# Optimization experiments

Measured on AMD Instinct MI355X. Metric: run time of the kernel, lower is better.

## Reference

```python
import jax, jax.numpy as jnp
import numpy as np

B, T, D = 8, 2048, 1024


def setup_inputs() -> dict:
    key = jax.random.key(0)
    ks = jax.random.split(key, 9)
    s = 1.0 / np.sqrt(D)
    return {
        "e": jax.random.normal(ks[0], (B, T, D), jnp.float32),
        "residual": jax.random.normal(ks[1], (B, T, D), jnp.float32),
        "Wq_w": jax.random.normal(ks[2], (D, D), jnp.float32) * s,
        "Wq_b": jax.random.normal(ks[3], (D,), jnp.float32) * s,
        "Wk_w": jax.random.normal(ks[4], (D, D), jnp.float32) * s,
        "Wk_b": jax.random.normal(ks[5], (D,), jnp.float32) * s,
        "Wv_w": jax.random.normal(ks[6], (D, D), jnp.float32) * s,
        "Wv_b": jax.random.normal(ks[7], (D,), jnp.float32) * s,
        "v_table": jax.random.normal(ks[8], (T, 1), jnp.float32),
    }


def reference(e, residual, Wq_w, Wq_b, Wk_w, Wk_b, Wv_w, Wv_b, v_table):
    T_ = e.shape[1]
    # relative position index: pos[i,j] = max(i - j, 0)
    pos = jnp.arange(T_)
    rel = jnp.maximum(pos[:, None] - pos[None, :], 0)          # (T, T) int
    pos_embd = v_table[rel, 0]                                 # (T, T) gather from Embedding(length, 1)

    # torch Linear: x @ W.T + b
    Q = e @ Wq_w.T + Wq_b                                      # (B, T, D)
    K = residual @ Wk_w.T + Wk_b                               # (B, T, D)
    V = e @ Wv_w.T + Wv_b                                      # (B, T, D)

    # Q @ K^T  (torch: Q @ Wk(residual).transpose(-2,-1))
    scores = jnp.einsum('btd,bsd->bts', Q, K)                  # (B, T, T)
    # einsum('BeT,Tt->BTt', K^T, pos_embd) == sum_e K[B,T,e] * pos_embd[T,t]
    scores = scores + K.sum(-1)[:, :, None] * pos_embd[None]   # (B, T, T)

    # causal mask via tril (zeros strictly-upper entries); NO softmax in this variant
    scores = scores * jnp.tril(jnp.ones((T_, T_), scores.dtype))
    return scores @ V                                          # (B, T, D)
```

## Files before the change

kernel.cpp:

```cpp
#include <hip/hip_runtime.h>

typedef unsigned short u16;
typedef __attribute__((ext_vector_type(8))) short bf16x8;
typedef __attribute__((ext_vector_type(8))) unsigned short u16x8;
typedef __attribute__((ext_vector_type(4))) float f32x4;

#define AS1 __attribute__((address_space(1)))
#define AS3 __attribute__((address_space(3)))

static __device__ __forceinline__ u16 f2bf(float f) {
  unsigned u = __float_as_uint(f);
  u += 0x7FFFu + ((u >> 16) & 1u);
  return (u16)(u >> 16);
}
static __device__ __forceinline__ float bf2f(u16 h) {
  return __uint_as_float(((unsigned)h) << 16);
}

__global__ __launch_bounds__(256) void conv_big(const float* __restrict__ e,
                                                const float* __restrict__ res,
                                                u16* __restrict__ eb, u16* __restrict__ rb) {
  int i = blockIdx.x * 256 + threadIdx.x;
  const float* in = blockIdx.z ? res : e;
  u16* out = blockIdx.z ? rb : eb;
  const float4* p = (const float4*)in + (size_t)i * 2;
  float4 a = p[0], b = p[1];
  u16x8 r;
  r[0] = f2bf(a.x); r[1] = f2bf(a.y); r[2] = f2bf(a.z); r[3] = f2bf(a.w);
  r[4] = f2bf(b.x); r[5] = f2bf(b.y); r[6] = f2bf(b.z); r[7] = f2bf(b.w);
  ((u16x8*)out)[i] = r;
}
__global__ __launch_bounds__(256) void conv_w(const float* __restrict__ w0,
                                              const float* __restrict__ w1,
                                              const float* __restrict__ w2,
                                              u16* __restrict__ o0, u16* __restrict__ o1,
                                              u16* __restrict__ o2,
                                              float* __restrict__ ksum) {
  int i = blockIdx.x * 256 + threadIdx.x;
  if (blockIdx.z == 3) {
    if (i < 16384) ksum[i] = 0.f;
    return;
  }
  const float* in = blockIdx.z == 0 ? w0 : (blockIdx.z == 1 ? w1 : w2);
  u16* out = blockIdx.z == 0 ? o0 : (blockIdx.z == 1 ? o1 : o2);
  const float4* p = (const float4*)in + (size_t)i * 2;
  float4 a = p[0], b = p[1];
  u16x8 r;
  r[0] = f2bf(a.x); r[1] = f2bf(a.y); r[2] = f2bf(a.z); r[3] = f2bf(a.w);
  r[4] = f2bf(b.x); r[5] = f2bf(b.y); r[6] = f2bf(b.z); r[7] = f2bf(b.w);
  ((u16x8*)out)[i] = r;
}

enum { M_BIASN = 0, M_BIASM = 1, M_SCORES = 2, M_OUT = 3 };

template <int MODE>
static __device__ __forceinline__ void core128(
    const u16* __restrict__ Ab, int lda, const u16* __restrict__ Bb, int ldb,
    char* smem, int m0, int n0, int nk, void* __restrict__ Cbase, int ldc,
    const float* __restrict__ bias, const float* __restrict__ ksb,
    const float* __restrict__ vtab, float* __restrict__ ksum_acc) {
  const int tid = threadIdx.x;
  const int lane = tid & 63;
  const int wid = tid >> 6;
  const int wm = wid >> 1, wn = wid & 1;

  char* As = smem;
  char* Bs = smem + 16384;

  const int rbase_st = tid >> 3;
  const int gcol = ((tid & 7) << 4) ^ ((rbase_st & 7) << 4);

  const int aoff = (wm * 64 + (lane & 15)) * 128;
  const int boff = (wn * 64 + (lane & 15)) * 128;
  const int c0 = ((0 * 4 + (lane >> 4)) ^ (lane & 7)) << 4;
  const int c1 = ((1 * 4 + (lane >> 4)) ^ (lane & 7)) << 4;

  f32x4 acc[4][4];
#pragma unroll
  for (int m = 0; m < 4; ++m)
#pragma unroll
    for (int n = 0; n < 4; ++n) acc[m][n] = (f32x4){0.f, 0.f, 0.f, 0.f};

  for (int kt = 0; kt < nk; ++kt) {
    const int k0 = kt * 64;
#pragma unroll
    for (int i = 0; i < 4; ++i) {
      const char* ga = (const char*)(Ab + (size_t)(m0 + i * 32 + rbase_st) * lda + k0) + gcol;
      __builtin_amdgcn_global_load_lds(
          (const AS1 void*)ga, (AS3 void*)(As + i * 4096 + wid * 1024), 16, 0, 0);
    }
#pragma unroll
    for (int i = 0; i < 4; ++i) {
      const char* gb = (const char*)(Bb + (size_t)(n0 + i * 32 + rbase_st) * ldb + k0) + gcol;
      __builtin_amdgcn_global_load_lds(
          (const AS1 void*)gb, (AS3 void*)(Bs + i * 4096 + wid * 1024), 16, 0, 0);
    }
    __syncthreads();
#pragma unroll
    for (int ks = 0; ks < 2; ++ks) {
      const int cks = ks ? c1 : c0;
      bf16x8 af[4], bfv[4];
#pragma unroll
      for (int m = 0; m < 4; ++m) af[m] = *(const bf16x8*)(As + aoff + m * 2048 + cks);
#pragma unroll
      for (int n = 0; n < 4; ++n) bfv[n] = *(const bf16x8*)(Bs + boff + n * 2048 + cks);
#pragma unroll
      for (int m = 0; m < 4; ++m)
#pragma unroll
        for (int n = 0; n < 4; ++n)
          acc[m][n] = __builtin_amdgcn_mfma_f32_16x16x32_bf16(af[m], bfv[n], acc[m][n], 0, 0, 0);
    }
    __syncthreads();
  }

  u16* C16 = (u16*)Cbase;
  float* Cf = (float*)Cbase;
  float rs[4][4];
  if (MODE == M_BIASN && ksum_acc) {
#pragma unroll
    for (int m = 0; m < 4; ++m)
#pragma unroll
      for (int j = 0; j < 4; ++j) rs[m][j] = 0.f;
  }
#pragma unroll
  for (int m = 0; m < 4; ++m) {
#pragma unroll
    for (int n = 0; n < 4; ++n) {
      const int rb = m0 + wm * 64 + m * 16 + ((lane >> 4) << 2);
      const int c = n0 + wn * 64 + n * 16 + (lane & 15);
#pragma unroll
      for (int j = 0; j < 4; ++j) {
        const int r = rb + j;
        float v = acc[m][n][j];
        if (MODE == M_BIASN) {
          v += bias[c];
          if (ksum_acc) rs[m][j] += v;
          C16[(size_t)r * ldc + c] = f2bf(v);
        } else if (MODE == M_BIASM) {
          v += bias[r];
          C16[(size_t)r * ldc + c] = f2bf(v);
        } else if (MODE == M_SCORES) {
          if (c <= r) v += ksb[r] * vtab[r - c];
          else v = 0.f;
          C16[(size_t)r * ldc + c] = f2bf(v);
        } else {
          Cf[(size_t)r * ldc + c] = v;
        }
      }
    }
  }
  if (MODE == M_BIASN && ksum_acc) {
#pragma unroll
    for (int m = 0; m < 4; ++m) {
      const int rb = m0 + wm * 64 + m * 16 + ((lane >> 4) << 2);
#pragma unroll
      for (int j = 0; j < 4; ++j) {
        float s = rs[m][j];
        s += __shfl_xor(s, 1);
        s += __shfl_xor(s, 2);
        s += __shfl_xor(s, 4);
        s += __shfl_xor(s, 8);
        if ((lane & 15) == 0) atomicAdd(&ksum_acc[rb + j], s);
      }
    }
  }
}

__global__ __launch_bounds__(256, 4) void k_qkv_proj(
    const u16* eb, const u16* rb, const u16* Wq, const u16* Wk, const u16* Wv,
    const float* bq, const float* bk, const float* bv,
    u16* Q, u16* K, u16* VT, float* ksum) {
  const int l = blockIdx.x;
  const int xcd = l & 7;
  const int idx = l >> 3;
  const int j = idx & 127;
  __shared__ char smem[32768];
  if (idx < 256) {
    const bool isK = idx >= 128;
    const int gy = xcd * 16 + (j >> 3);
    const int gx = j & 7;
    core128<M_BIASN>(isK ? rb : eb, 1024, isK ? Wk : Wq, 1024, smem,
                     gy * 128, gx * 128, 16, isK ? K : Q, 1024,
                     isK ? bk : bq, nullptr, nullptr, isK ? ksum : nullptr);
  } else {
    const int gxt = xcd * 16 + (j >> 3);
    const int gyd = j & 7;
    core128<M_BIASM>(Wv, 1024, eb, 1024, smem, gyd * 128, gxt * 128, 16,
                     VT, 16384, bv, nullptr, nullptr, nullptr);
  }
}
__global__ __launch_bounds__(256, 4) void k_scores(
    const u16* Q, const u16* K, u16* S, const float* ksum, const float* vtab) {
  const int l = blockIdx.x;
  const int z = l & 7;
  const int h = l >> 3;
  int gy = 0;
#pragma unroll
  for (int q = 1; q < 16; ++q) if (q * (q + 1) / 2 <= h) gy = q;
  const int gx = h - gy * (gy + 1) / 2;
  __shared__ char smem[32768];
  core128<M_SCORES>(Q + (size_t)z * 2048 * 1024, 1024,
                    K + (size_t)z * 2048 * 1024, 1024, smem,
                    gy * 128, gx * 128, 16,
                    S + (size_t)z * 2048 * 2048, 2048,
                    nullptr, ksum + (size_t)z * 2048, vtab, nullptr);
}
__global__ __launch_bounds__(256, 4) void k_out(
    const u16* S, const u16* VT, float* O) {
  const int l = blockIdx.x;
  const int z = l & 7;
  const int idx = l >> 3;
  const int gy = 15 - (idx >> 3);
  const int gx = idx & 7;
  const int nk = (gy + 1) * 2;
  __shared__ char smem[32768];
  core128<M_OUT>(S + (size_t)z * 2048 * 2048, 2048,
                 VT + (size_t)z * 2048, 16384, smem,
                 gy * 128, gx * 128, nk,
                 O + (size_t)z * 2048 * 1024, 1024,
                 nullptr, nullptr, nullptr, nullptr);
}

extern "C" void kernel_launch(void* const* d_in, const int* in_sizes, int n_in,
                              void* d_out, int out_size, void* d_ws, size_t ws_size,
                              hipStream_t stream) {
  (void)in_sizes; (void)n_in; (void)out_size; (void)ws_size;
  const float* e    = (const float*)d_in[0];
  const float* res  = (const float*)d_in[1];
  const float* Wq_w = (const float*)d_in[2];
  const float* Wq_b = (const float*)d_in[3];
  const float* Wk_w = (const float*)d_in[4];
  const float* Wk_b = (const float*)d_in[5];
  const float* Wv_w = (const float*)d_in[6];
  const float* Wv_b = (const float*)d_in[7];
  const float* vtab = (const float*)d_in[8];

  char* ws = (char*)d_ws;
  const size_t SZ = 33554432;
  u16* ebf = (u16*)(ws);
  u16* rbf = (u16*)(ws + SZ);
  u16* Qb  = (u16*)(ws + 2 * SZ);
  u16* Kb  = (u16*)(ws + 3 * SZ);
  u16* VT  = (u16*)(ws + 4 * SZ);
  u16* Wqb = (u16*)(ws + 5 * SZ);
  u16* Wkb = (u16*)(ws + 5 * SZ + 2097152);
  u16* Wvb = (u16*)(ws + 5 * SZ + 2 * 2097152);
  float* ksum = (float*)(ws + 5 * SZ + 3 * 2097152);
  u16* scores = (u16*)(ws);

  conv_big<<<dim3(8192, 1, 2), 256, 0, stream>>>(e, res, ebf, rbf);
  conv_w<<<dim3(512, 1, 4), 256, 0, stream>>>(Wq_w, Wk_w, Wv_w, Wqb, Wkb, Wvb, ksum);

  k_qkv_proj<<<dim3(3072, 1, 1), 256, 0, stream>>>(ebf, rbf, Wqb, Wkb, Wvb,
                                                   Wq_b, Wk_b, Wv_b, Qb, Kb, VT, ksum);

  k_scores<<<dim3(1088, 1, 1), 256, 0, stream>>>(Qb, Kb, scores, ksum, vtab);

  k_out<<<dim3(1024, 1, 1), 256, 0, stream>>>(scores, VT, (float*)d_out);
}
```

Baseline: 250.8 us.

## Fuse scores and output GEMMs into persistent kernel with atomic work queue

Replaces the separate scores and output kernels with one persistent kernel. Blocks pull tiles from a per-batch atomic queue: score tiles come first, in reverse row order. Output tiles spin-wait on per-row completion counters, so the output GEMM for finished rows can start while other rows' scores are still being computed. This removes the tail and launch gap between the two phases, at the cost of atomics, spin-waiting, and a risk of deadlock if waiting blocks starve the producers. The control counters are zeroed in the weight-conversion kernel.

```diff
diff --git a/kernel.cpp b/kernel.cpp
--- a/kernel.cpp
+++ b/kernel.cpp
@@ -12,9 +12,6 @@
   unsigned u = __float_as_uint(f);
   u += 0x7FFFu + ((u >> 16) & 1u);
   return (u16)(u >> 16);
-}
-static __device__ __forceinline__ float bf2f(u16 h) {
-  return __uint_as_float(((unsigned)h) << 16);
 }
 
 __global__ __launch_bounds__(256) void conv_big(const float* __restrict__ e,
@@ -39,6 +36,7 @@
   int i = blockIdx.x * 256 + threadIdx.x;
   if (blockIdx.z == 3) {
     if (i < 16384) ksum[i] = 0.f;
+    else if (i < 16384 + 136) ((int*)(ksum + 16384))[i - 16384] = 0;
     return;
   }
   const float* in = blockIdx.z == 0 ? w0 : (blockIdx.z == 1 ? w1 : w2);
@@ -189,36 +187,57 @@
                      VT, 16384, bv, nullptr, nullptr, nullptr);
   }
 }
-__global__ __launch_bounds__(256, 4) void k_scores(
-    const u16* Q, const u16* K, u16* S, const float* ksum, const float* vtab) {
-  const int l = blockIdx.x;
-  const int z = l & 7;
-  const int h = l >> 3;
-  int gy = 0;
-#pragma unroll
-  for (int q = 1; q < 16; ++q) if (q * (q + 1) / 2 <= h) gy = q;
-  const int gx = h - gy * (gy + 1) / 2;
+
+__global__ __launch_bounds__(256, 4) void k_att(
+    const u16* Q, const u16* K, const u16* VT, u16* S, float* O,
+    const float* ksum, const float* vtab, int* ctrl) {
+  const int z = blockIdx.x & 7;
+  int* rowcnt = ctrl;
+  int* queue = ctrl + 128;
   __shared__ char smem[32768];
-  core128<M_SCORES>(Q + (size_t)z * 2048 * 1024, 1024,
-                    K + (size_t)z * 2048 * 1024, 1024, smem,
-                    gy * 128, gx * 128, 16,
-                    S + (size_t)z * 2048 * 2048, 2048,
-                    nullptr, ksum + (size_t)z * 2048, vtab, nullptr);
-}
-__global__ __launch_bounds__(256, 4) void k_out(
-    const u16* S, const u16* VT, float* O) {
-  const int l = blockIdx.x;
-  const int z = l & 7;
-  const int idx = l >> 3;
-  const int gy = 15 - (idx >> 3);
-  const int gx = idx & 7;
-  const int nk = (gy + 1) * 2;
-  __shared__ char smem[32768];
-  core128<M_OUT>(S + (size_t)z * 2048 * 2048, 2048,
-                 VT + (size_t)z * 2048, 16384, smem,
-                 gy * 128, gx * 128, nk,
-                 O + (size_t)z * 2048 * 1024, 1024,
-                 nullptr, nullptr, nullptr, nullptr);
+  __shared__ int s_t;
+  for (;;) {
+    __syncthreads();
+    if (threadIdx.x == 0)
+      s_t = __hip_atomic_fetch_add(&queue[z], 1, __ATOMIC_RELAXED,
+                                   __HIP_MEMORY_SCOPE_AGENT);
+    __syncthreads();
+    const int t = s_t;
+    if (t >= 264) break;
+    if (t < 136) {
+      const int hp = 135 - t;
+      int gy = 0;
+#pragma unroll
+      for (int q = 1; q < 16; ++q) if (q * (q + 1) / 2 <= hp) gy = q;
+      const int gx = hp - gy * (gy + 1) / 2;
+      core128<M_SCORES>(Q + (size_t)z * 2048 * 1024, 1024,
+                        K + (size_t)z * 2048 * 1024, 1024, smem,
+                        gy * 128, gx * 128, 16,
+                        S + (size_t)z * 2048 * 2048, 2048,
+                        nullptr, ksum + (size_t)z * 2048, vtab, nullptr);
+      __threadfence();
+      __syncthreads();
+      if (threadIdx.x == 0)
+        __hip_atomic_fetch_add(&rowcnt[z * 16 + gy], 1, __ATOMIC_RELEASE,
+                               __HIP_MEMORY_SCOPE_AGENT);
+    } else {
+      const int u = t - 136;
+      const int gy = 15 - (u >> 3);
+      const int gx = u & 7;
+      if (threadIdx.x == 0) {
+        while (__hip_atomic_load(&rowcnt[z * 16 + gy], __ATOMIC_ACQUIRE,
+                                 __HIP_MEMORY_SCOPE_AGENT) < gy + 1)
+          __builtin_amdgcn_s_sleep(2);
+      }
+      __syncthreads();
+      __threadfence();
+      core128<M_OUT>(S + (size_t)z * 2048 * 2048, 2048,
+                     VT + (size_t)z * 2048, 16384, smem,
+                     gy * 128, gx * 128, (gy + 1) * 2,
+                     O + (size_t)z * 2048 * 1024, 1024,
+                     nullptr, nullptr, nullptr, nullptr);
+    }
+  }
 }
 
 extern "C" void kernel_launch(void* const* d_in, const int* in_sizes, int n_in,
@@ -246,6 +265,7 @@
   u16* Wkb = (u16*)(ws + 5 * SZ + 2097152);
   u16* Wvb = (u16*)(ws + 5 * SZ + 2 * 2097152);
   float* ksum = (float*)(ws + 5 * SZ + 3 * 2097152);
+  int* ctrl = (int*)(ksum + 16384);
   u16* scores = (u16*)(ws);
 
   conv_big<<<dim3(8192, 1, 2), 256, 0, stream>>>(e, res, ebf, rbf);
@@ -254,7 +274,6 @@
   k_qkv_proj<<<dim3(3072, 1, 1), 256, 0, stream>>>(ebf, rbf, Wqb, Wkb, Wvb,
                                                    Wq_b, Wk_b, Wv_b, Qb, Kb, VT, ksum);
 
-  k_scores<<<dim3(1088, 1, 1), 256, 0, stream>>>(Qb, Kb, scores, ksum, vtab);
-
-  k_out<<<dim3(1024, 1, 1), 256, 0, stream>>>(scores, VT, (float*)d_out);
-}
+  k_att<<<dim3(1024, 1, 1), 256, 0, stream>>>(Qb, Kb, VT, scores, (float*)d_out,
+                                              ksum, vtab, ctrl);
+}
```

New measurement: 711.9 us. 184% more time.
